# Performance work log

Hardware: AMD Instinct MI355X
Metric: run time of the kernel (lower is better)

The kernel has to match this reference:

```python
import jax, jax.numpy as jnp
import numpy as np
import math

N = 131072   # number of points
C = 32       # embed_dim
K = 19       # num_class
ZD = 16      # z_dim
BN_EPS = 1e-4
SIG_THR = 0.8


def setup_inputs():
    key = jax.random.key(0)
    ks = jax.random.split(key, 16)
    f32 = jnp.float32
    rn = lambda k, s, sc=1.0: jax.random.normal(k, s, dtype=f32) * sc
    return {
        'feat': rn(ks[0], (N, C)),
        'scene_flow': rn(ks[1], (N, 3)),
        'coarse_pred': rn(ks[2], (N, K)),
        'z': rn(ks[3], (ZD,)),
        'select_w1': rn(ks[4], (C, C), 0.2),
        'bn_gamma': jnp.ones((C,), f32),
        'bn_beta': jnp.zeros((C,), f32),
        'bn_mean': jnp.zeros((C,), f32),
        'bn_var': jnp.ones((C,), f32),
        'select_w2': rn(ks[5], (C, 1), 0.2),
        'select_b2': jnp.zeros((1,), f32),
        'wq': rn(ks[6], (C, C), 0.2), 'bq': jnp.zeros((C,), f32),
        'wk': rn(ks[7], (C, C), 0.2), 'bk': jnp.zeros((C,), f32),
        'wv': rn(ks[8], (C, C), 0.2), 'bv': jnp.zeros((C,), f32),
        'wo': rn(ks[9], (C, C), 0.2), 'bo': jnp.zeros((C,), f32),
        'wt': rn(ks[10], (2 * C, C), 0.2), 'bt': jnp.zeros((C,), f32),
        'w_out': rn(ks[11], (C, K), 0.2), 'b_out': jnp.zeros((K,), f32),
        'w_gen': rn(ks[12], (ZD + K + 3, C), 0.2), 'b_gen': jnp.zeros((C,), f32),
    }


def _forward(feat, scene_flow, coarse_pred, z, select_w1, bn_gamma, bn_beta,
             bn_mean, bn_var, select_w2, select_b2, wq, bq, wk, bk, wv, bv,
             wo, bo, wt, bt, w_out, b_out, w_gen, b_gen):
    cp = jax.nn.softmax(coarse_pred, axis=-1)                      # (N, K)
    temp_mask = jnp.any(scene_flow != 0, axis=-1)                  # (N,)
    # select_mlp: Linear(no bias) -> BatchNorm(eval, eps=1e-4) -> ReLU -> Linear -> Sigmoid
    h = (feat @ select_w1 - bn_mean) / jnp.sqrt(bn_var + BN_EPS) * bn_gamma + bn_beta
    h = jnp.maximum(h, 0.0)
    score = jax.nn.sigmoid(h @ select_w2 + select_b2)[:, 0]        # (N,)
    valid = (score < SIG_THR) & temp_mask                          # (N,)
    # cvae stand-in: linear over concat(z, onehot(class), scene_flow) -> (N, K, C)
    wz, wc, ws = w_gen[:ZD], w_gen[ZD:ZD + K], w_gen[ZD + K:]
    gen = (z @ wz + b_gen)[None, None, :] + wc[None, :, :] + (scene_flow @ ws)[:, None, :]
    gen = gen * cp[:, :, None]                                     # scale by softmax prob
    # tiny cross-attention: 1 query per point over K=19 class prototypes
    q = feat @ wq + bq                                             # (N, C)
    k_ = jnp.einsum('nkc,cd->nkd', gen, wk) + bk                   # (N, K, C)
    v_ = jnp.einsum('nkc,cd->nkd', gen, wv) + bv                   # (N, K, C)
    attn = jax.nn.softmax(jnp.einsum('nd,nkd->nk', q, k_) / math.sqrt(C), axis=-1)
    aug = jnp.einsum('nk,nkd->nd', attn, v_) @ wo + bo             # (N, C)
    # scatter-back: invalid points get zeros (equivalent to torch boolean scatter)
    new_feat = jnp.where(valid[:, None], aug, 0.0)
    refine = jnp.concatenate([feat, new_feat], axis=-1) @ wt + bt  # (N, C)
    return refine @ w_out + b_out                                  # (N, K)


def reference(feat, scene_flow, coarse_pred, z, select_w1, bn_gamma, bn_beta,
              bn_mean, bn_var, select_w2, select_b2, wq, bq, wk, bk, wv, bv,
              wo, bo, wt, bt, w_out, b_out, w_gen, b_gen):
    return _forward(feat, scene_flow, coarse_pred, z, select_w1, bn_gamma,
                    bn_beta, bn_mean, bn_var, select_w2, select_b2, wq, bq,
                    wk, bk, wv, bv, wo, bo, wt, bt, w_out, b_out, w_gen, b_gen)
```

## Files before the change

### kernel.cpp

```cpp
#include <hip/hip_runtime.h>

#define NPTS 131072

constexpr int OFF_SW1 = 0;
constexpr int OFF_BNS = 1024;
constexpr int OFF_BNH = 1056;
constexpr int OFF_SW2 = 1088;
constexpr int OFF_B2  = 1120;
constexpr int OFF_QG  = 1121;
constexpr int OFF_QGB = 1729;
constexpr int OFF_QM  = 1748;
constexpr int OFF_QMB = 1844;
constexpr int OFF_QBV = 1847;
constexpr int OFF_QBB = 1879;
constexpr int OFF_A1  = 1880;
constexpr int OFF_GVB = 2488;
constexpr int OFF_MVB = 2849;
constexpr int OFF_CV  = 2906;
constexpr int OFF_BB  = 2925;

#define CONST_AS __attribute__((address_space(4)))
__device__ __forceinline__ const CONST_AS float* to_const(const float* p) {
    return (const CONST_AS float*)p;
}

__global__ __launch_bounds__(256) void precompute_k(
    const float* __restrict__ z,
    const float* __restrict__ sw1,
    const float* __restrict__ bn_gamma,
    const float* __restrict__ bn_beta,
    const float* __restrict__ bn_mean,
    const float* __restrict__ bn_var,
    const float* __restrict__ sw2,
    const float* __restrict__ sb2,
    const float* __restrict__ wq, const float* __restrict__ bq,
    const float* __restrict__ wk, const float* __restrict__ bk,
    const float* __restrict__ wv, const float* __restrict__ bv,
    const float* __restrict__ wo, const float* __restrict__ bo,
    const float* __restrict__ wt, const float* __restrict__ bt,
    const float* __restrict__ wout, const float* __restrict__ bout,
    const float* __restrict__ wgen, const float* __restrict__ bgen,
    float* __restrict__ W)
{
    __shared__ float Lwk[1024], Lwv[1024], Lwq[1024], Lwo[1024];
    __shared__ float Lwt[2048], Lwout[608], Lwgen[1632];
    __shared__ float LG[608], LGk[608], LGv[608], LMk[96], LMv[96];
    __shared__ float LA2[608], LB[608], Lg0[32];

    const int t = threadIdx.x;

    for (int i = t; i < 1024; i += 256) {
        Lwk[i] = wk[i]; Lwv[i] = wv[i];
        Lwq[i] = wq[i]; Lwo[i] = wo[i];
    }
    for (int i = t; i < 2048; i += 256) Lwt[i] = wt[i];
    for (int i = t; i < 608;  i += 256) Lwout[i] = wout[i];
    for (int i = t; i < 1632; i += 256) Lwgen[i] = wgen[i];
    __syncthreads();

    if (t < 32) {
        float g = bgen[t];
        for (int d = 0; d < 16; ++d) g += z[d] * Lwgen[d*32 + t];
        Lg0[t] = g;
        float scale = bn_gamma[t] / sqrtf(bn_var[t] + 1e-4f);
        W[OFF_BNS + t] = scale;
        W[OFF_BNH + t] = bn_beta[t] - bn_mean[t] * scale;
        W[OFF_SW2 + t] = sw2[t];
    }
    if (t == 0) W[OFF_B2] = sb2[0];
    for (int i = t; i < 1024; i += 256) W[OFF_SW1 + i] = sw1[(i & 31)*32 + (i >> 5)];
    for (int i = t; i < 96; i += 256) {
        int m = i >> 5, c = i & 31;
        float a = 0.f, b = 0.f;
        for (int e = 0; e < 32; ++e) {
            float wsrow = Lwgen[(35 + m)*32 + e];
            a += wsrow * Lwk[e*32 + c];
            b += wsrow * Lwv[e*32 + c];
        }
        LMk[i] = a; LMv[i] = b;
    }
    for (int i = t; i < 608; i += 256) {
        int e = i / 19, j = i % 19;
        float a1 = 0.f, a2 = 0.f;
        for (int d = 0; d < 32; ++d) {
            float w_ = Lwout[d*19 + j];
            a1 += Lwt[e*32 + d] * w_;
            a2 += Lwt[(32 + e)*32 + d] * w_;
        }
        W[OFF_A1 + i] = a1; LA2[e*19 + j] = a2;
    }
    for (int i = t; i < 19; i += 256) {
        float a = bout[i];
        for (int d = 0; d < 32; ++d) a += bt[d] * Lwout[d*19 + i];
        W[OFF_BB + i] = a;
    }
    for (int i = t; i < 32; i += 256) {
        float a = 0.f;
        for (int c = 0; c < 32; ++c) a += Lwq[i*32 + c] * bk[c];
        W[OFF_QBV + i] = a;
    }
    if (t == 0) {
        float a = 0.f;
        for (int c = 0; c < 32; ++c) a += bq[c] * bk[c];
        W[OFF_QBB] = a;
    }
    __syncthreads();

    for (int i = t; i < 608; i += 256) {
        int k = i >> 5, e = i & 31;
        LG[i] = Lg0[e] + Lwgen[(16 + k)*32 + e];
    }
    __syncthreads();

    for (int i = t; i < 608; i += 256) {
        int k = i >> 5, c = i & 31;
        float a = 0.f, b = 0.f;
        for (int e = 0; e < 32; ++e) {
            float g = LG[k*32 + e];
            a += g * Lwk[e*32 + c];
            b += g * Lwv[e*32 + c];
        }
        LGk[i] = a; LGv[i] = b;
    }
    for (int i = t; i < 608; i += 256) {
        int c = i / 19, j = i % 19;
        float a = 0.f;
        for (int d = 0; d < 32; ++d) a += Lwo[c*32 + d] * LA2[d*19 + j];
        LB[i] = a;
    }
    for (int i = t; i < 96; i += 256) {
        int e = i / 3, m = i % 3;
        float a = 0.f;
        for (int c = 0; c < 32; ++c) a += Lwq[e*32 + c] * LMk[m*32 + c];
        W[OFF_QM + i] = a;
    }
    if (t < 3) {
        float a = 0.f;
        for (int c = 0; c < 32; ++c) a += bq[c] * LMk[t*32 + c];
        W[OFF_QMB + t] = a;
    }
    __syncthreads();

    for (int i = t; i < 608; i += 256) {
        int e = i / 19, k = i % 19;
        float a = 0.f;
        for (int c = 0; c < 32; ++c) a += Lwq[e*32 + c] * LGk[k*32 + c];
        W[OFF_QG + i] = a;
    }
    for (int i = t; i < 19; i += 256) {
        float a = 0.f;
        for (int c = 0; c < 32; ++c) a += bq[c] * LGk[i*32 + c];
        W[OFF_QGB + i] = a;
    }
    for (int i = t; i < 361; i += 256) {
        int k = i / 19, j = i % 19;
        float a = 0.f;
        for (int c = 0; c < 32; ++c) a += LGv[k*32 + c] * LB[c*19 + j];
        W[OFF_GVB + i] = a;
    }
    for (int i = t; i < 57; i += 256) {
        int m = i / 19, j = i % 19;
        float a = 0.f;
        for (int c = 0; c < 32; ++c) a += LMv[m*32 + c] * LB[c*19 + j];
        W[OFF_MVB + i] = a;
    }
    for (int i = t; i < 19; i += 256) {
        float a = 0.f;
        for (int c = 0; c < 32; ++c) a += bv[c] * LB[c*19 + i];
        for (int d = 0; d < 32; ++d) a += bo[d] * LA2[d*19 + i];
        W[OFF_CV + i] = a;
    }
}

__global__ __launch_bounds__(256, 1) void main_k(
    const float* __restrict__ feat,
    const float* __restrict__ sflow,
    const float* __restrict__ cpred,
    const float* __restrict__ Wg,
    float* __restrict__ out)
{
    const CONST_AS float* W = to_const(Wg);
    const int n = blockIdx.x * 256 + threadIdx.x;

    float f[32];
    const float4* fp = (const float4*)(feat + (long)n * 32);
#pragma unroll
    for (int g = 0; g < 8; ++g) {
        float4 v = fp[g];
        f[g*4+0] = v.x; f[g*4+1] = v.y; f[g*4+2] = v.z; f[g*4+3] = v.w;
    }

    float s0 = sflow[(long)n*3 + 0];
    float s1 = sflow[(long)n*3 + 1];
    float s2 = sflow[(long)n*3 + 2];
    bool tmask = (s0 != 0.f) | (s1 != 0.f) | (s2 != 0.f);

    float cp[19];
#pragma unroll
    for (int k = 0; k < 19; ++k) cp[k] = cpred[(long)n*19 + k];
    float m1 = cp[0];
#pragma unroll
    for (int k = 1; k < 19; ++k) m1 = fmaxf(m1, cp[k]);
    float sum1 = 0.f;
#pragma unroll
    for (int k = 0; k < 19; ++k) { cp[k] = __expf(cp[k] - m1); sum1 += cp[k]; }
    float r1 = 1.f / sum1;
#pragma unroll
    for (int k = 0; k < 19; ++k) cp[k] *= r1;

    float sacc = W[OFF_B2];
#pragma unroll
    for (int c = 0; c < 32; ++c) {
        float a = 0.f;
#pragma unroll
        for (int e = 0; e < 32; ++e) a = fmaf(f[e], W[OFF_SW1 + c*32 + e], a);
        float h = fmaf(a, W[OFF_BNS + c], W[OFF_BNH + c]);
        h = fmaxf(h, 0.f);
        sacc = fmaf(h, W[OFF_SW2 + c], sacc);
    }
    bool valid = tmask && (sacc < 1.3862943611198906f);

    float qg[19];
#pragma unroll
    for (int k = 0; k < 19; ++k) qg[k] = W[OFF_QGB + k];
    float qm0 = W[OFF_QMB + 0], qm1 = W[OFF_QMB + 1], qm2 = W[OFF_QMB + 2];
    float qb = W[OFF_QBB];
#pragma unroll
    for (int e = 0; e < 32; ++e) {
        float fe = f[e];
#pragma unroll
        for (int k = 0; k < 19; ++k) qg[k] = fmaf(fe, W[OFF_QG + e*19 + k], qg[k]);
        qm0 = fmaf(fe, W[OFF_QM + e*3 + 0], qm0);
        qm1 = fmaf(fe, W[OFF_QM + e*3 + 1], qm1);
        qm2 = fmaf(fe, W[OFF_QM + e*3 + 2], qm2);
        qb  = fmaf(fe, W[OFF_QBV + e], qb);
    }
    float qs = s0*qm0 + s1*qm1 + s2*qm2;

    const float RS = 0.17677669529663687f;
    float l[19];
#pragma unroll
    for (int k = 0; k < 19; ++k) l[k] = fmaf(cp[k], qg[k] + qs, qb) * RS;

    float m2 = l[0];
#pragma unroll
    for (int k = 1; k < 19; ++k) m2 = fmaxf(m2, l[k]);
    float sum2 = 0.f;
#pragma unroll
    for (int k = 0; k < 19; ++k) { l[k] = __expf(l[k] - m2); sum2 += l[k]; }
    float r2 = 1.f / sum2;
    float Sw = 0.f;
#pragma unroll
    for (int k = 0; k < 19; ++k) { l[k] = l[k] * r2 * cp[k]; Sw += l[k]; }

    float o[19];
#pragma unroll
    for (int j = 0; j < 19; ++j) o[j] = W[OFF_BB + j];
#pragma unroll
    for (int e = 0; e < 32; ++e) {
        float fe = f[e];
#pragma unroll
        for (int j = 0; j < 19; ++j) o[j] = fmaf(fe, W[OFF_A1 + e*19 + j], o[j]);
    }

    float a2[19];
#pragma unroll
    for (int j = 0; j < 19; ++j) a2[j] = W[OFF_CV + j];
    float c0 = Sw * s0, c1 = Sw * s1, c2 = Sw * s2;
#pragma unroll
    for (int j = 0; j < 19; ++j) a2[j] = fmaf(c0, W[OFF_MVB + j], a2[j]);
#pragma unroll
    for (int j = 0; j < 19; ++j) a2[j] = fmaf(c1, W[OFF_MVB + 19 + j], a2[j]);
#pragma unroll
    for (int j = 0; j < 19; ++j) a2[j] = fmaf(c2, W[OFF_MVB + 38 + j], a2[j]);
#pragma unroll
    for (int k = 0; k < 19; ++k) {
        float lk = l[k];
#pragma unroll
        for (int j = 0; j < 19; ++j) a2[j] = fmaf(lk, W[OFF_GVB + k*19 + j], a2[j]);
    }

    float vg = valid ? 1.f : 0.f;
    float* op = out + (long)n * 19;
#pragma unroll
    for (int j = 0; j < 19; ++j) op[j] = fmaf(vg, a2[j], o[j]);
}

extern "C" void kernel_launch(void* const* d_in, const int* in_sizes, int n_in,
                              void* d_out, int out_size, void* d_ws, size_t ws_size,
                              hipStream_t stream) {
    const float* feat  = (const float*)d_in[0];
    const float* sflow = (const float*)d_in[1];
    const float* cpred = (const float*)d_in[2];
    const float* z     = (const float*)d_in[3];
    const float* sw1   = (const float*)d_in[4];
    const float* bn_g  = (const float*)d_in[5];
    const float* bn_b  = (const float*)d_in[6];
    const float* bn_m  = (const float*)d_in[7];
    const float* bn_v  = (const float*)d_in[8];
    const float* sw2   = (const float*)d_in[9];
    const float* sb2   = (const float*)d_in[10];
    const float* wq    = (const float*)d_in[11];
    const float* bq    = (const float*)d_in[12];
    const float* wk    = (const float*)d_in[13];
    const float* bk    = (const float*)d_in[14];
    const float* wv    = (const float*)d_in[15];
    const float* bv    = (const float*)d_in[16];
    const float* wo    = (const float*)d_in[17];
    const float* bo    = (const float*)d_in[18];
    const float* wt    = (const float*)d_in[19];
    const float* bt    = (const float*)d_in[20];
    const float* wout  = (const float*)d_in[21];
    const float* bout  = (const float*)d_in[22];
    const float* wgen  = (const float*)d_in[23];
    const float* bgen  = (const float*)d_in[24];

    float* W = (float*)d_ws;

    hipLaunchKernelGGL(precompute_k, dim3(1), dim3(256), 0, stream,
                       z, sw1, bn_g, bn_b, bn_m, bn_v, sw2, sb2,
                       wq, bq, wk, bk, wv, bv, wo, bo, wt, bt,
                       wout, bout, wgen, bgen, W);

    hipLaunchKernelGGL(main_k, dim3(NPTS / 256), dim3(256), 0, stream,
                       feat, sflow, cpred, W, (float*)d_out);
}
```

Baseline: 171.7 us.

## Split single-block weight precompute into three multi-block kernels

Result: faster. 165.7 us (-3.5%).

```diff
diff --git a/kernel.cpp b/kernel.cpp
--- a/kernel.cpp
+++ b/kernel.cpp
@@ -18,157 +18,150 @@
 constexpr int OFF_MVB = 2849;
 constexpr int OFF_CV  = 2906;
 constexpr int OFF_BB  = 2925;
+constexpr int XG   = 3072;
+constexpr int XA2  = 3680;
+constexpr int XMK  = 4288;
+constexpr int XMV  = 4384;
+constexpr int XGK  = 4480;
+constexpr int XGV  = 5088;
+constexpr int XB   = 5696;
 
 #define CONST_AS __attribute__((address_space(4)))
 __device__ __forceinline__ const CONST_AS float* to_const(const float* p) {
     return (const CONST_AS float*)p;
 }
 
-__global__ __launch_bounds__(256) void precompute_k(
+__global__ __launch_bounds__(256) void pre_a(
     const float* __restrict__ z,
     const float* __restrict__ sw1,
-    const float* __restrict__ bn_gamma,
-    const float* __restrict__ bn_beta,
-    const float* __restrict__ bn_mean,
-    const float* __restrict__ bn_var,
-    const float* __restrict__ sw2,
-    const float* __restrict__ sb2,
+    const float* __restrict__ bn_gamma, const float* __restrict__ bn_beta,
+    const float* __restrict__ bn_mean,  const float* __restrict__ bn_var,
+    const float* __restrict__ sw2,      const float* __restrict__ sb2,
     const float* __restrict__ wq, const float* __restrict__ bq,
     const float* __restrict__ wk, const float* __restrict__ bk,
-    const float* __restrict__ wv, const float* __restrict__ bv,
-    const float* __restrict__ wo, const float* __restrict__ bo,
+    const float* __restrict__ wv,
     const float* __restrict__ wt, const float* __restrict__ bt,
     const float* __restrict__ wout, const float* __restrict__ bout,
     const float* __restrict__ wgen, const float* __restrict__ bgen,
     float* __restrict__ W)
 {
-    __shared__ float Lwk[1024], Lwv[1024], Lwq[1024], Lwo[1024];
-    __shared__ float Lwt[2048], Lwout[608], Lwgen[1632];
-    __shared__ float LG[608], LGk[608], LGv[608], LMk[96], LMv[96];
-    __shared__ float LA2[608], LB[608], Lg0[32];
-
-    const int t = threadIdx.x;
-
-    for (int i = t; i < 1024; i += 256) {
-        Lwk[i] = wk[i]; Lwv[i] = wv[i];
-        Lwq[i] = wq[i]; Lwo[i] = wo[i];
-    }
-    for (int i = t; i < 2048; i += 256) Lwt[i] = wt[i];
-    for (int i = t; i < 608;  i += 256) Lwout[i] = wout[i];
-    for (int i = t; i < 1632; i += 256) Lwgen[i] = wgen[i];
-    __syncthreads();
-
-    if (t < 32) {
-        float g = bgen[t];
-        for (int d = 0; d < 16; ++d) g += z[d] * Lwgen[d*32 + t];
-        Lg0[t] = g;
+    int i = blockIdx.x * 256 + threadIdx.x;
+    if (i < 1024) {
+        W[OFF_SW1 + i] = sw1[(i & 31) * 32 + (i >> 5)];
+    } else if (i < 1632) {
+        int t = i - 1024, e = t / 19, j = t % 19;
+        float a1 = 0.f, a2 = 0.f;
+        for (int d = 0; d < 32; ++d) {
+            float w_ = wout[d*19 + j];
+            a1 += wt[e*32 + d] * w_;
+            a2 += wt[(32 + e)*32 + d] * w_;
+        }
+        W[OFF_A1 + t] = a1; W[XA2 + t] = a2;
+    } else if (i < 2240) {
+        int t = i - 1632, k = t >> 5, e = t & 31;
+        float g = bgen[e];
+        for (int d = 0; d < 16; ++d) g += z[d] * wgen[d*32 + e];
+        W[XG + t] = g + wgen[(16 + k)*32 + e];
+    } else if (i < 2336) {
+        int t = i - 2240, m = t >> 5, c = t & 31;
+        float a = 0.f, b = 0.f;
+        for (int e = 0; e < 32; ++e) {
+            float wsr = wgen[(35 + m)*32 + e];
+            a += wsr * wk[e*32 + c];
+            b += wsr * wv[e*32 + c];
+        }
+        W[XMK + t] = a; W[XMV + t] = b;
+    } else if (i < 2368) {
+        int t = i - 2336;
         float scale = bn_gamma[t] / sqrtf(bn_var[t] + 1e-4f);
         W[OFF_BNS + t] = scale;
         W[OFF_BNH + t] = bn_beta[t] - bn_mean[t] * scale;
         W[OFF_SW2 + t] = sw2[t];
-    }
-    if (t == 0) W[OFF_B2] = sb2[0];
-    for (int i = t; i < 1024; i += 256) W[OFF_SW1 + i] = sw1[(i & 31)*32 + (i >> 5)];
-    for (int i = t; i < 96; i += 256) {
-        int m = i >> 5, c = i & 31;
-        float a = 0.f, b = 0.f;
-        for (int e = 0; e < 32; ++e) {
-            float wsrow = Lwgen[(35 + m)*32 + e];
-            a += wsrow * Lwk[e*32 + c];
-            b += wsrow * Lwv[e*32 + c];
-        }
-        LMk[i] = a; LMv[i] = b;
-    }
-    for (int i = t; i < 608; i += 256) {
-        int e = i / 19, j = i % 19;
-        float a1 = 0.f, a2 = 0.f;
-        for (int d = 0; d < 32; ++d) {
-            float w_ = Lwout[d*19 + j];
-            a1 += Lwt[e*32 + d] * w_;
-            a2 += Lwt[(32 + e)*32 + d] * w_;
-        }
-        W[OFF_A1 + i] = a1; LA2[e*19 + j] = a2;
-    }
-    for (int i = t; i < 19; i += 256) {
-        float a = bout[i];
-        for (int d = 0; d < 32; ++d) a += bt[d] * Lwout[d*19 + i];
-        W[OFF_BB + i] = a;
-    }
-    for (int i = t; i < 32; i += 256) {
-        float a = 0.f;
-        for (int c = 0; c < 32; ++c) a += Lwq[i*32 + c] * bk[c];
-        W[OFF_QBV + i] = a;
-    }
-    if (t == 0) {
+    } else if (i < 2387) {
+        int t = i - 2368;
+        float a = bout[t];
+        for (int d = 0; d < 32; ++d) a += bt[d] * wout[d*19 + t];
+        W[OFF_BB + t] = a;
+    } else if (i < 2419) {
+        int t = i - 2387;
+        float a = 0.f;
+        for (int c = 0; c < 32; ++c) a += wq[t*32 + c] * bk[c];
+        W[OFF_QBV + t] = a;
+    } else if (i == 2419) {
+        W[OFF_B2] = sb2[0];
+    } else if (i == 2420) {
         float a = 0.f;
         for (int c = 0; c < 32; ++c) a += bq[c] * bk[c];
         W[OFF_QBB] = a;
     }
-    __syncthreads();
-
-    for (int i = t; i < 608; i += 256) {
-        int k = i >> 5, e = i & 31;
-        LG[i] = Lg0[e] + Lwgen[(16 + k)*32 + e];
-    }
-    __syncthreads();
-
-    for (int i = t; i < 608; i += 256) {
+}
+
+__global__ __launch_bounds__(256) void pre_b(
+    const float* __restrict__ wq, const float* __restrict__ bq,
+    const float* __restrict__ wk, const float* __restrict__ wv,
+    const float* __restrict__ wo,
+    float* __restrict__ W)
+{
+    int i = blockIdx.x * 256 + threadIdx.x;
+    if (i < 608) {
         int k = i >> 5, c = i & 31;
         float a = 0.f, b = 0.f;
         for (int e = 0; e < 32; ++e) {
-            float g = LG[k*32 + e];
-            a += g * Lwk[e*32 + c];
-            b += g * Lwv[e*32 + c];
+            float g = W[XG + k*32 + e];
+            a += g * wk[e*32 + c];
+            b += g * wv[e*32 + c];
         }
-        LGk[i] = a; LGv[i] = b;
-    }
-    for (int i = t; i < 608; i += 256) {
-        int c = i / 19, j = i % 19;
-        float a = 0.f;
-        for (int d = 0; d < 32; ++d) a += Lwo[c*32 + d] * LA2[d*19 + j];
-        LB[i] = a;
-    }
-    for (int i = t; i < 96; i += 256) {
-        int e = i / 3, m = i % 3;
-        float a = 0.f;
-        for (int c = 0; c < 32; ++c) a += Lwq[e*32 + c] * LMk[m*32 + c];
-        W[OFF_QM + i] = a;
-    }
-    if (t < 3) {
-        float a = 0.f;
-        for (int c = 0; c < 32; ++c) a += bq[c] * LMk[t*32 + c];
-        W[OFF_QMB + t] = a;
-    }
-    __syncthreads();
-
-    for (int i = t; i < 608; i += 256) {
+        W[XGK + i] = a; W[XGV + i] = b;
+    } else if (i < 1216) {
+        int t = i - 608, c = t / 19, j = t % 19;
+        float a = 0.f;
+        for (int d = 0; d < 32; ++d) a += wo[c*32 + d] * W[XA2 + d*19 + j];
+        W[XB + t] = a;
+    } else if (i < 1312) {
+        int t = i - 1216, e = t / 3, m = t % 3;
+        float a = 0.f;
+        for (int c = 0; c < 32; ++c) a += wq[e*32 + c] * W[XMK + m*32 + c];
+        W[OFF_QM + t] = a;
+    } else if (i < 1315) {
+        int m = i - 1312;
+        float a = 0.f;
+        for (int c = 0; c < 32; ++c) a += bq[c] * W[XMK + m*32 + c];
+        W[OFF_QMB + m] = a;
+    }
+}
+
+__global__ __launch_bounds__(256) void pre_c(
+    const float* __restrict__ wq, const float* __restrict__ bq,
+    const float* __restrict__ bv, const float* __restrict__ bo,
+    float* __restrict__ W)
+{
+    int i = blockIdx.x * 256 + threadIdx.x;
+    if (i < 608) {
         int e = i / 19, k = i % 19;
         float a = 0.f;
-        for (int c = 0; c < 32; ++c) a += Lwq[e*32 + c] * LGk[k*32 + c];
+        for (int c = 0; c < 32; ++c) a += wq[e*32 + c] * W[XGK + k*32 + c];
         W[OFF_QG + i] = a;
-    }
-    for (int i = t; i < 19; i += 256) {
-        float a = 0.f;
-        for (int c = 0; c < 32; ++c) a += bq[c] * LGk[i*32 + c];
-        W[OFF_QGB + i] = a;
-    }
-    for (int i = t; i < 361; i += 256) {
-        int k = i / 19, j = i % 19;
-        float a = 0.f;
-        for (int c = 0; c < 32; ++c) a += LGv[k*32 + c] * LB[c*19 + j];
-        W[OFF_GVB + i] = a;
-    }
-    for (int i = t; i < 57; i += 256) {
-        int m = i / 19, j = i % 19;
-        float a = 0.f;
-        for (int c = 0; c < 32; ++c) a += LMv[m*32 + c] * LB[c*19 + j];
-        W[OFF_MVB + i] = a;
-    }
-    for (int i = t; i < 19; i += 256) {
-        float a = 0.f;
-        for (int c = 0; c < 32; ++c) a += bv[c] * LB[c*19 + i];
-        for (int d = 0; d < 32; ++d) a += bo[d] * LA2[d*19 + i];
-        W[OFF_CV + i] = a;
+    } else if (i < 627) {
+        int k = i - 608;
+        float a = 0.f;
+        for (int c = 0; c < 32; ++c) a += bq[c] * W[XGK + k*32 + c];
+        W[OFF_QGB + k] = a;
+    } else if (i < 988) {
+        int t = i - 627, k = t / 19, j = t % 19;
+        float a = 0.f;
+        for (int c = 0; c < 32; ++c) a += W[XGV + k*32 + c] * W[XB + c*19 + j];
+        W[OFF_GVB + t] = a;
+    } else if (i < 1045) {
+        int t = i - 988, m = t / 19, j = t % 19;
+        float a = 0.f;
+        for (int c = 0; c < 32; ++c) a += W[XMV + m*32 + c] * W[XB + c*19 + j];
+        W[OFF_MVB + t] = a;
+    } else if (i < 1064) {
+        int j = i - 1045;
+        float a = 0.f;
+        for (int c = 0; c < 32; ++c) a += bv[c] * W[XB + c*19 + j];
+        for (int d = 0; d < 32; ++d) a += bo[d] * W[XA2 + d*19 + j];
+        W[OFF_CV + j] = a;
     }
 }
 
@@ -317,10 +310,13 @@
 
     float* W = (float*)d_ws;
 
-    hipLaunchKernelGGL(precompute_k, dim3(1), dim3(256), 0, stream,
+    hipLaunchKernelGGL(pre_a, dim3(10), dim3(256), 0, stream,
                        z, sw1, bn_g, bn_b, bn_m, bn_v, sw2, sb2,
-                       wq, bq, wk, bk, wv, bv, wo, bo, wt, bt,
-                       wout, bout, wgen, bgen, W);
+                       wq, bq, wk, bk, wv, wt, bt, wout, bout, wgen, bgen, W);
+    hipLaunchKernelGGL(pre_b, dim3(6), dim3(256), 0, stream,
+                       wq, bq, wk, wv, wo, W);
+    hipLaunchKernelGGL(pre_c, dim3(5), dim3(256), 0, stream,
+                       wq, bq, bv, bo, W);
 
     hipLaunchKernelGGL(main_k, dim3(NPTS / 256), dim3(256), 0, stream,
                        feat, sflow, cpred, W, (float*)d_out);
```
